# Optimization experiments

Hardware: AMD Instinct MI355X
Metric: run time of the kernel (lower is better)

Reference implementation:

```python
import jax, jax.numpy as jnp
import numpy as np

N_QUBITS = 14
N_LAYERS = 2          # n_ansatz_layers
N_TIMESTEPS = 4
DEGREE = 2
N_ROTS = 4 * N_QUBITS * N_LAYERS  # 448 rotation params per qnode call
DIM = 2 ** N_QUBITS
BSZ = 256
STATE_DIM = 4
OUT_DIM = 2


def apply_ry(state, wire, theta):
    # state: (B, 2^n) complex64; theta: (B,) float. Wire 0 = most significant bit (PennyLane convention).
    L, R = 2 ** wire, 2 ** (N_QUBITS - wire - 1)
    st = state.reshape(-1, L, 2, R)
    c = jnp.cos(theta * 0.5)[:, None, None]
    s = jnp.sin(theta * 0.5)[:, None, None]
    s0, s1 = st[:, :, 0, :], st[:, :, 1, :]
    new = jnp.stack([c * s0 - s * s1, s * s0 + c * s1], axis=2)
    return new.reshape(state.shape)


def apply_crx(state, ctrl, tgt, theta):
    # Controlled-RX: RX(theta) on tgt when ctrl bit is 1.
    a, b = (ctrl, tgt) if ctrl < tgt else (tgt, ctrl)
    La, Lm, Lr = 2 ** a, 2 ** (b - a - 1), 2 ** (N_QUBITS - b - 1)
    st = state.reshape(-1, La, 2, Lm, 2, Lr)
    c = jnp.cos(theta * 0.5)[:, None, None, None]
    s = jnp.sin(theta * 0.5)[:, None, None, None]
    if ctrl < tgt:
        # axis2 = ctrl, axis4 = tgt
        ctl1 = st[:, :, 1]                      # (B, La, Lm, 2, Lr)
        t0, t1 = ctl1[:, :, :, 0, :], ctl1[:, :, :, 1, :]
        n0 = c * t0 - 1j * s * t1
        n1 = -1j * s * t0 + c * t1
        new_ctl1 = jnp.stack([n0, n1], axis=3)
        out = jnp.stack([st[:, :, 0], new_ctl1], axis=2)
    else:
        # axis2 = tgt, axis4 = ctrl
        t0c1, t1c1 = st[:, :, 0, :, 1, :], st[:, :, 1, :, 1, :]
        n0 = c * t0c1 - 1j * s * t1c1
        n1 = -1j * s * t0c1 + c * t1c1
        new_t0 = jnp.stack([st[:, :, 0, :, 0, :], n0], axis=3)
        new_t1 = jnp.stack([st[:, :, 1, :, 0, :], n1], axis=3)
        out = jnp.stack([new_t0, new_t1], axis=2)
    return out.reshape(state.shape)


def sim14(state, params):
    # sim14_circuit: per layer -> RY ring, descending CRX ring [i,(i+1)%n], RY ring, CRX ring [i,(i-1)%n].
    idx = 0
    for _ in range(N_LAYERS):
        for i in range(N_QUBITS):
            state = apply_ry(state, i, params[:, idx]); idx += 1
        for i in range(N_QUBITS - 1, -1, -1):
            state = apply_crx(state, i, (i + 1) % N_QUBITS, params[:, idx]); idx += 1
        for i in range(N_QUBITS):
            state = apply_ry(state, i, params[:, idx]); idx += 1
        for i in [N_QUBITS - 1] + list(range(N_QUBITS - 1)):
            state = apply_crx(state, i, (i - 1) % N_QUBITS, params[:, idx]); idx += 1
    return state


def poly_state(base, tparams, mix_coeffs, poly_coeffs):
    # evaluate_polynomial_state_pl: degree+1 rounds of timestep-mixed circuit outputs.
    result = jnp.zeros_like(base)
    for d in range(DEGREE + 1):
        mixed = jnp.zeros_like(base)
        for t in range(N_TIMESTEPS):
            mixed = mixed + mix_coeffs[:, t:t + 1] * sim14(base, tparams[:, t, :])
        result = result + poly_coeffs[d] * mixed
        if d < DEGREE:
            nrm = jnp.linalg.norm(mixed, axis=1, keepdims=True)
            base = mixed / (nrm + 1e-9)
    return result


def expval_z(state, wire):
    L, R = 2 ** wire, 2 ** (N_QUBITS - wire - 1)
    st = state.reshape(-1, L, 2, R)
    p = jnp.sum(jnp.abs(st) ** 2, axis=(1, 3))  # (B, 2)
    return p[:, 0] - p[:, 1]


def setup_inputs() -> dict:
    key = jax.random.key(0)
    ks = jax.random.split(key, 7)
    return {
        "x": jax.random.normal(ks[0], (BSZ, STATE_DIM), dtype=jnp.float32),
        "W_in": jax.random.normal(ks[1], (STATE_DIM, N_TIMESTEPS * N_ROTS), dtype=jnp.float32) * 0.3,
        "b_in": jax.random.normal(ks[2], (N_TIMESTEPS * N_ROTS,), dtype=jnp.float32) * 0.1,
        "mix_coeffs": jax.random.normal(ks[3], (1, N_TIMESTEPS), dtype=jnp.float32) * 0.5,
        "poly_coeffs": jax.random.normal(ks[4], (DEGREE + 1,), dtype=jnp.float32) * 0.5,
        "W_out": jax.random.normal(ks[5], (N_QUBITS, OUT_DIM), dtype=jnp.float32) * 0.3,
        "b_out": jax.random.normal(ks[6], (OUT_DIM,), dtype=jnp.float32) * 0.1,
    }


def reference(x, W_in, b_in, mix_coeffs, poly_coeffs, W_out, b_out):
    bsz = x.shape[0]
    # v1-style sigmoid [0,1] angle scaling
    angles = jax.nn.sigmoid(x @ W_in + b_in)                # (B, T*n_rots)
    tparams = angles.reshape(bsz, N_TIMESTEPS, N_ROTS)
    base = jnp.zeros((bsz, DIM), dtype=jnp.complex64).at[:, 0].set(1.0)
    final = poly_state(base, tparams, mix_coeffs, poly_coeffs)
    final = final / (jnp.linalg.norm(final, axis=1, keepdims=True) + 1e-9)
    expz = jnp.stack([expval_z(final, w) for w in range(N_QUBITS)], axis=1)  # (B, n_qubits) real
    return expz.astype(jnp.float32) @ W_out + b_out
```

## Files before the change

### kernel.cpp

```cpp
#include <hip/hip_runtime.h>
#include <math.h>

#define DIM 16384
#define NTH 512
#define NBLK 256
#define F4 (DIM / 2)

typedef float v2f __attribute__((ext_vector_type(2)));
typedef float v4f __attribute__((ext_vector_type(4)));

__host__ __device__ constexpr int cswz(int i) {
  return i ^ ((i >> 4) & 15) ^ ((i >> 8) & 15) ^ ((i >> 12) & 3);
}

constexpr int LW[8][5] = {
  {13, 12, 11, 10, 0}, {10, 9, 8, 7, 6}, {6, 5, 4, 3, 2}, {2, 1, 0, 3, 4},
  {12, 13, 0, 1, 2}, {2, 3, 4, 5, 6}, {6, 7, 8, 9, 10}, {10, 11, 12, 13, 9},
};
constexpr int PMAP[8][9] = {
  {4, 5, 6, 7, 8, 9, 10, 11, 12}, {0, 1, 2, 11, 8, 9, 10, 12, 13},
  {0, 1, 2, 3, 4, 5, 6, 12, 13}, {0, 1, 2, 3, 4, 5, 6, 7, 8},
  {2, 3, 4, 5, 6, 7, 8, 9, 10}, {0, 1, 2, 3, 4, 5, 6, 12, 13},
  {0, 1, 2, 11, 8, 9, 10, 12, 13}, {5, 6, 7, 8, 9, 10, 11, 12, 13},
};
constexpr int NG[8] = {9, 8, 8, 3, 9, 8, 8, 3};
constexpr int GATES[8][9][4] = {
  {{0,4,0,0},{0,3,0,10},{0,2,0,11},{0,1,0,12},{0,0,0,13},{1,0,4,14},{1,1,0,15},{1,2,1,16},{1,3,2,17}},
  {{0,4,0,6},{0,3,0,7},{0,2,0,8},{0,1,0,9},{1,1,0,18},{1,2,1,19},{1,3,2,20},{1,4,3,21},{0,0,0,0}},
  {{0,4,0,2},{0,3,0,3},{0,2,0,4},{0,1,0,5},{1,1,0,22},{1,2,1,23},{1,3,2,24},{1,4,3,25},{0,0,0,0}},
  {{0,1,0,1},{1,1,0,26},{1,2,1,27},{0,0,0,0},{0,0,0,0},{0,0,0,0},{0,0,0,0},{0,0,0,0},{0,0,0,0}},
  {{0,2,0,28},{0,3,0,29},{0,4,0,30},{0,0,0,40},{0,1,0,41},{1,1,0,42},{1,2,1,43},{1,3,2,44},{1,4,3,45}},
  {{0,1,0,31},{0,2,0,32},{0,3,0,33},{0,4,0,34},{1,1,0,46},{1,2,1,47},{1,3,2,48},{1,4,3,49},{0,0,0,0}},
  {{0,1,0,35},{0,2,0,36},{0,3,0,37},{0,4,0,38},{1,1,0,50},{1,2,1,51},{1,3,2,52},{1,4,3,53},{0,0,0,0}},
  {{0,1,0,39},{1,1,0,54},{1,2,1,55},{0,0,0,0},{0,0,0,0},{0,0,0,0},{0,0,0,0},{0,0,0,0},{0,0,0,0}},
};
__host__ __device__ constexpr int offcube5(int p, int j) {
  int o = 0;
  for (int b = 0; b < 5; ++b)
    if ((j >> b) & 1) o |= 1 << (13 - LW[p][b]);
  return o;
}

template <int PID, int MODE>
__device__ __forceinline__ void fb_pass(v2f* __restrict__ S, const v2f* __restrict__ CS,
                                        int lb, int tid, v2f* __restrict__ a) {
  int base = 0;
#pragma unroll
  for (int k = 0; k < 9; ++k) base |= ((tid >> k) & 1) << PMAP[PID][k];
  const int sb = cswz(base);
  if (MODE == 1) {
#pragma unroll
    for (int j = 0; j < 32; ++j) a[j] = v2f{0.f, 0.f};
    if (tid == 0) a[0] = v2f{1.f, 0.f};
  } else {
#pragma unroll
    for (int j = 0; j < 32; ++j) a[j] = S[sb ^ cswz(offcube5(PID, j))];
  }
#pragma unroll
  for (int g = 0; g < NG[PID]; ++g) {
    const v2f cs2 = CS[lb + GATES[PID][g][3]];
    const float c = cs2.x, s = cs2.y;
    if (GATES[PID][g][0] == 0) {
      const int tb = GATES[PID][g][1];
#pragma unroll
      for (int j = 0; j < 32; ++j)
        if (!((j >> tb) & 1)) {
          const int j2 = j | (1 << tb);
          const v2f a0 = a[j], a1 = a[j2];
          a[j]  = c * a0 - s * a1;
          a[j2] = s * a0 + c * a1;
        }
    } else {
      const int bc = GATES[PID][g][1], bt = GATES[PID][g][2];
#pragma unroll
      for (int j = 0; j < 32; ++j)
        if (((j >> bc) & 1) && !((j >> bt) & 1)) {
          const int j2 = j | (1 << bt);
          const v2f t0 = a[j], t1 = a[j2];
          a[j]  = c * t0 + s * v2f{t1.y, -t1.x};
          a[j2] = c * t1 + s * v2f{t0.y, -t0.x};
        }
    }
  }
  if (MODE != 2) {
#pragma unroll
    for (int j = 0; j < 32; ++j) S[sb ^ cswz(offcube5(PID, j))] = a[j];
  }
  __syncthreads();
}

__device__ __forceinline__ void sim16(v2f* __restrict__ S, const v2f* __restrict__ CS,
                                      int tid, bool init0) {
  v2f a[32];
  if (init0) fb_pass<0, 1>(S, CS, 0, tid, a);
  else       fb_pass<0, 0>(S, CS, 0, tid, a);
  fb_pass<1, 0>(S, CS, 0, tid, a);
  fb_pass<2, 0>(S, CS, 0, tid, a);
  fb_pass<3, 0>(S, CS, 0, tid, a);
  fb_pass<4, 0>(S, CS, 0, tid, a);
  fb_pass<5, 0>(S, CS, 0, tid, a);
  fb_pass<6, 0>(S, CS, 0, tid, a);
  fb_pass<7, 0>(S, CS, 0, tid, a);
  fb_pass<0, 0>(S, CS, 56, tid, a);
  fb_pass<1, 0>(S, CS, 56, tid, a);
  fb_pass<2, 0>(S, CS, 56, tid, a);
  fb_pass<3, 0>(S, CS, 56, tid, a);
  fb_pass<4, 0>(S, CS, 56, tid, a);
  fb_pass<5, 0>(S, CS, 56, tid, a);
  fb_pass<6, 0>(S, CS, 56, tid, a);
  fb_pass<7, 0>(S, CS, 56, tid, a);
}

__device__ __forceinline__ float block_sum(float v, int tid, float* red) {
#pragma unroll
  for (int off = 32; off; off >>= 1) v += __shfl_xor(v, off);
  if ((tid & 63) == 0) red[tid >> 6] = v;
  __syncthreads();
  float tot = 0.f;
#pragma unroll
  for (int w = 0; w < 8; ++w) tot += red[w];
  __syncthreads();
  return tot;
}

__global__ __launch_bounds__(NTH, 1) void qts_kernel(
    const float* __restrict__ x, const float* __restrict__ Win,
    const float* __restrict__ bin, const float* __restrict__ mix,
    const float* __restrict__ poly, const float* __restrict__ Wout,
    const float* __restrict__ bout, float* __restrict__ out,
    v4f* __restrict__ gAall, v4f* __restrict__ gBall) {
  __shared__ v2f S[DIM + 448 + 128];
  v4f* SF = (v4f*)S;
  v2f* CSall = S + DIM;
  float* red = (float*)(S + DIM + 448);
  const int tid = threadIdx.x;
  const int b = blockIdx.x;
  v4f* gA = gAall + (size_t)b * F4;
  v4f* gB = gBall + (size_t)b * F4;

  if (tid < 448) {
    float z = bin[tid];
    const float x0 = x[b * 4 + 0], x1 = x[b * 4 + 1], x2 = x[b * 4 + 2], x3 = x[b * 4 + 3];
    z += x0 * Win[tid] + x1 * Win[448 + tid] + x2 * Win[896 + tid] + x3 * Win[1344 + tid];
    const float th = 1.f / (1.f + expf(-z));
    float sn, cc;
    sincosf(0.5f * th, &sn, &cc);
    CSall[tid] = v2f{cc, sn};
  }
  __syncthreads();

  const float p0 = poly[0], p1 = poly[1], p2 = poly[2];
  float n1 = 0.f, n2 = 0.f;

  for (int t = 0; t < 4; ++t) {
    sim16(S, CSall + t * 112, tid, true);
    const float mc = mix[t];
    if (t == 0) {
#pragma unroll
      for (int j = 0; j < 16; ++j) { const int f = tid + j * NTH; gA[f] = mc * SF[f]; }
    } else if (t < 3) {
#pragma unroll
      for (int j = 0; j < 16; ++j) { const int f = tid + j * NTH; gA[f] += mc * SF[f]; }
    } else {
      float part = 0.f;
#pragma unroll
      for (int j = 0; j < 16; ++j) {
        const int f = tid + j * NTH;
        const v4f v = gA[f] + mc * SF[f];
        gA[f] = v; SF[f] = v;
        part += v.x * v.x + v.y * v.y + v.z * v.z + v.w * v.w;
      }
      n1 = sqrtf(block_sum(part, tid, red));
    }
    __syncthreads();
  }
  const float n1e = n1 + 1e-9f;
  const float c2 = p1 / n1e;

  for (int t = 0; t < 4; ++t) {
    sim16(S, CSall + t * 112, tid, false);
    const float mc = mix[t];
    if (t == 0) {
#pragma unroll
      for (int j = 0; j < 16; ++j) {
        const int f = tid + j * NTH;
        gB[f] = mc * SF[f]; SF[f] = gA[f];
      }
    } else if (t < 3) {
#pragma unroll
      for (int j = 0; j < 16; ++j) {
        const int f = tid + j * NTH;
        gB[f] += mc * SF[f]; SF[f] = gA[f];
      }
    } else {
      float part = 0.f;
#pragma unroll
      for (int j = 0; j < 16; ++j) {
        const int f = tid + j * NTH;
        const v4f v = gB[f] + mc * SF[f];
        gB[f] = v;
        gA[f] = p0 * gA[f] + c2 * v;
        SF[f] = v;
        part += v.x * v.x + v.y * v.y + v.z * v.z + v.w * v.w;
      }
      n2 = sqrtf(block_sum(part, tid, red));
    }
    __syncthreads();
  }
  const float n2e = n2 + 1e-9f * n1e;
  const float c3 = p2 / n2e;

  float part15[15];
#pragma unroll
  for (int v = 0; v < 15; ++v) part15[v] = 0.f;
  for (int t = 0; t < 4; ++t) {
    sim16(S, CSall + t * 112, tid, false);
    const float mc = c3 * mix[t];
    if (t < 3) {
#pragma unroll
      for (int j = 0; j < 16; ++j) {
        const int f = tid + j * NTH;
        gA[f] += mc * SF[f]; SF[f] = gB[f];
      }
      __syncthreads();
    } else {
#pragma unroll
      for (int j = 0; j < 16; ++j) {
        const int f = tid + j * NTH;
        const v4f r = gA[f] + mc * SF[f];
        const int i0 = cswz(2 * f);
        const int i1 = i0 ^ 1;
        const float pa = r.x * r.x + r.y * r.y;
        const float pb = r.z * r.z + r.w * r.w;
        part15[14] += pa + pb;
#pragma unroll
        for (int w = 0; w < 14; ++w) {
          part15[w] += ((i0 >> (13 - w)) & 1) ? -pa : pa;
          part15[w] += ((i1 >> (13 - w)) & 1) ? -pb : pb;
        }
      }
      __syncthreads();
    }
  }

#pragma unroll
  for (int v = 0; v < 15; ++v) {
    float xv = part15[v];
#pragma unroll
    for (int off = 32; off; off >>= 1) xv += __shfl_xor(xv, off);
    if ((tid & 63) == 0) red[(tid >> 6) * 15 + v] = xv;
  }
  __syncthreads();
  if (tid < 15) {
    float tot = 0.f;
#pragma unroll
    for (int w = 0; w < 8; ++w) tot += red[w * 15 + tid];
    red[128 + tid] = tot;
  }
  __syncthreads();
  if (tid < 2) {
    const float nrm = sqrtf(red[128 + 14]) + 1e-9f;
    const float iv = 1.f / (nrm * nrm);
    float o = bout[tid];
#pragma unroll
    for (int w = 0; w < 14; ++w) o += red[128 + w] * iv * Wout[w * 2 + tid];
    out[b * 2 + tid] = o;
  }
}

__device__ __forceinline__ void fb_sim(v2f* __restrict__ S, const v2f* __restrict__ CS,
                                       int tid, v2f* __restrict__ a,
                                       const v2f* __restrict__ basev, int own_sb,
                                       bool initzero) {
  if (initzero) {
    fb_pass<0, 1>(S, CS, 0, tid, a);
  } else {
#pragma unroll
    for (int j = 0; j < 32; ++j) S[own_sb ^ cswz(offcube5(7, j))] = basev[j];
    __syncthreads();
    fb_pass<0, 0>(S, CS, 0, tid, a);
  }
  fb_pass<1, 0>(S, CS, 0, tid, a);
  fb_pass<2, 0>(S, CS, 0, tid, a);
  fb_pass<3, 0>(S, CS, 0, tid, a);
  fb_pass<4, 0>(S, CS, 0, tid, a);
  fb_pass<5, 0>(S, CS, 0, tid, a);
  fb_pass<6, 0>(S, CS, 0, tid, a);
  fb_pass<7, 0>(S, CS, 0, tid, a);
  fb_pass<0, 0>(S, CS, 56, tid, a);
  fb_pass<1, 0>(S, CS, 56, tid, a);
  fb_pass<2, 0>(S, CS, 56, tid, a);
  fb_pass<3, 0>(S, CS, 56, tid, a);
  fb_pass<4, 0>(S, CS, 56, tid, a);
  fb_pass<5, 0>(S, CS, 56, tid, a);
  fb_pass<6, 0>(S, CS, 56, tid, a);
  fb_pass<7, 2>(S, CS, 56, tid, a);
}
__global__ __launch_bounds__(NTH, 1) void qts_fb(
    const float* __restrict__ x, const float* __restrict__ Win,
    const float* __restrict__ bin, const float* __restrict__ mix,
    const float* __restrict__ poly, const float* __restrict__ Wout,
    const float* __restrict__ bout, float* __restrict__ out) {
  __shared__ v2f S[DIM + 448 + 128];
  v2f* CSall = S + DIM;
  float* red = (float*)(S + DIM + 448);
  const int tid = threadIdx.x;
  const int b = blockIdx.x;
  if (tid < 448) {
    float z = bin[tid];
    const float x0 = x[b * 4 + 0], x1 = x[b * 4 + 1], x2 = x[b * 4 + 2], x3 = x[b * 4 + 3];
    z += x0 * Win[tid] + x1 * Win[448 + tid] + x2 * Win[896 + tid] + x3 * Win[1344 + tid];
    const float th = 1.f / (1.f + expf(-z));
    float sn, cc;
    sincosf(0.5f * th, &sn, &cc);
    CSall[tid] = v2f{cc, sn};
  }
  __syncthreads();
  int ownbase = 0;
#pragma unroll
  for (int k = 0; k < 9; ++k) ownbase |= ((tid >> k) & 1) << PMAP[7][k];
  const int own_sb = cswz(ownbase);
  const float p0 = poly[0], p1 = poly[1], p2 = poly[2];
  v2f a[32], acc[32], basev[32];
  float alpha;
#pragma unroll
  for (int j = 0; j < 32; ++j) acc[j] = v2f{0.f, 0.f};
  for (int t = 0; t < 4; ++t) {
    fb_sim(S, CSall + t * 112, tid, a, basev, own_sb, true);
    const float mc = mix[t];
#pragma unroll
    for (int j = 0; j < 32; ++j) acc[j] += mc * a[j];
  }
  {
    float part = 0.f;
#pragma unroll
    for (int j = 0; j < 32; ++j) part += acc[j].x * acc[j].x + acc[j].y * acc[j].y;
    const float tot = block_sum(part, tid, red);
    const float nu = sqrtf(tot) + 1e-9f;
    const float inv = 1.f / nu;
    alpha = p0 * nu;
#pragma unroll
    for (int j = 0; j < 32; ++j) { basev[j] = inv * acc[j]; acc[j] = v2f{0.f, 0.f}; }
  }
  for (int t = 0; t < 4; ++t) {
    fb_sim(S, CSall + t * 112, tid, a, basev, own_sb, false);
    const float mc = mix[t];
#pragma unroll
    for (int j = 0; j < 32; ++j) acc[j] += mc * a[j];
  }
  {
    float part = 0.f;
#pragma unroll
    for (int j = 0; j < 32; ++j) part += acc[j].x * acc[j].x + acc[j].y * acc[j].y;
    const float tot = block_sum(part, tid, red);
    const float nu = sqrtf(tot) + 1e-9f;
    const float inv = 1.f / nu;
#pragma unroll
    for (int j = 0; j < 32; ++j) {
      const v2f tmp = acc[j];
      acc[j] = alpha * basev[j] + p1 * tmp;
      basev[j] = inv * tmp;
    }
  }
  for (int t = 0; t < 4; ++t) {
    fb_sim(S, CSall + t * 112, tid, a, basev, own_sb, false);
    const float mc = p2 * mix[t];
#pragma unroll
    for (int j = 0; j < 32; ++j) acc[j] += mc * a[j];
  }
  float part[15];
#pragma unroll
  for (int v = 0; v < 15; ++v) part[v] = 0.f;
#pragma unroll
  for (int j = 0; j < 32; ++j) {
    const int idx = ownbase | offcube5(7, j);
    const float p = acc[j].x * acc[j].x + acc[j].y * acc[j].y;
    part[14] += p;
#pragma unroll
    for (int w = 0; w < 14; ++w) part[w] += ((idx >> (13 - w)) & 1) ? -p : p;
  }
  __syncthreads();
#pragma unroll
  for (int v = 0; v < 15; ++v) {
    float xv = part[v];
#pragma unroll
    for (int off = 32; off; off >>= 1) xv += __shfl_xor(xv, off);
    if ((tid & 63) == 0) red[(tid >> 6) * 15 + v] = xv;
  }
  __syncthreads();
  if (tid < 15) {
    float tot = 0.f;
#pragma unroll
    for (int w = 0; w < 8; ++w) tot += red[w * 15 + tid];
    red[128 + tid] = tot;
  }
  __syncthreads();
  if (tid < 2) {
    const float nrm = sqrtf(red[128 + 14]) + 1e-9f;
    const float iv = 1.f / (nrm * nrm);
    float o = bout[tid];
#pragma unroll
    for (int w = 0; w < 14; ++w) o += red[128 + w] * iv * Wout[w * 2 + tid];
    out[b * 2 + tid] = o;
  }
}

extern "C" void kernel_launch(void* const* d_in, const int* in_sizes, int n_in,
                              void* d_out, int out_size, void* d_ws, size_t ws_size,
                              hipStream_t stream) {
  const float* x    = (const float*)d_in[0];
  const float* Win  = (const float*)d_in[1];
  const float* bin  = (const float*)d_in[2];
  const float* mix  = (const float*)d_in[3];
  const float* poly = (const float*)d_in[4];
  const float* Wout = (const float*)d_in[5];
  const float* bout = (const float*)d_in[6];
  float* out = (float*)d_out;

  const size_t need = 2ull * NBLK * F4 * sizeof(v4f);
  if (ws_size >= need) {
    v4f* gA = (v4f*)d_ws;
    v4f* gB = gA + (size_t)NBLK * F4;
    qts_kernel<<<NBLK, NTH, 0, stream>>>(x, Win, bin, mix, poly, Wout, bout, out, gA, gB);
  } else {
    qts_fb<<<NBLK, NTH, 0, stream>>>(x, Win, bin, mix, poly, Wout, bout, out);
  }
}
```

Before: 967.1 us.

## Use 1024 threads per block with 4-qubit register passes in main kernel

The main kernel now runs 1024 threads per block. Each thread holds 16 amplitudes (4 local qubits) instead of 32 (5 local qubits), and the gate schedule is regrouped into 10 passes per layer instead of 8. This raises wave-level parallelism per CU and lowers register pressure, since only one block of 256 fits each CU. The cost is more shared-memory round trips and more __syncthreads barriers per circuit. The fallback kernel keeps the old 512-thread, 5-qubit scheme under renamed tables.

Result: no change. 962.6 us (-0.5%).

```diff
diff --git a/kernel.cpp b/kernel.cpp
--- a/kernel.cpp
+++ b/kernel.cpp
@@ -2,9 +2,10 @@
 #include <math.h>
 
 #define DIM 16384
-#define NTH 512
+#define NTH 1024
 #define NBLK 256
 #define F4 (DIM / 2)
+#define IT4 (F4 / NTH)
 
 typedef float v2f __attribute__((ext_vector_type(2)));
 typedef float v4f __attribute__((ext_vector_type(4)));
@@ -13,57 +14,66 @@
   return i ^ ((i >> 4) & 15) ^ ((i >> 8) & 15) ^ ((i >> 12) & 3);
 }
 
-constexpr int LW[8][5] = {
-  {13, 12, 11, 10, 0}, {10, 9, 8, 7, 6}, {6, 5, 4, 3, 2}, {2, 1, 0, 3, 4},
-  {12, 13, 0, 1, 2}, {2, 3, 4, 5, 6}, {6, 7, 8, 9, 10}, {10, 11, 12, 13, 9},
+constexpr int LWp[10][4] = {
+  {13, 0, 12, 11}, {10, 9, 8, 11}, {7, 6, 5, 8}, {4, 3, 2, 5}, {1, 0, 2, 3},
+  {13, 12, 0, 1}, {2, 1, 3, 4}, {5, 4, 6, 7}, {8, 7, 9, 10}, {11, 10, 12, 9},
 };
-constexpr int PMAP[8][9] = {
-  {4, 5, 6, 7, 8, 9, 10, 11, 12}, {0, 1, 2, 11, 8, 9, 10, 12, 13},
-  {0, 1, 2, 3, 4, 5, 6, 12, 13}, {0, 1, 2, 3, 4, 5, 6, 7, 8},
-  {2, 3, 4, 5, 6, 7, 8, 9, 10}, {0, 1, 2, 3, 4, 5, 6, 12, 13},
-  {0, 1, 2, 11, 8, 9, 10, 12, 13}, {5, 6, 7, 8, 9, 10, 11, 12, 13},
+constexpr int PM[10][10] = {
+  {3, 4, 5, 6, 7, 8, 9, 10, 11, 12},
+  {0, 1, 6, 7, 8, 9, 10, 11, 12, 13},
+  {0, 1, 2, 3, 4, 9, 10, 11, 12, 13},
+  {0, 1, 2, 3, 4, 5, 6, 7, 12, 13},
+  {0, 1, 2, 3, 4, 5, 6, 7, 8, 9},
+  {2, 3, 4, 5, 6, 7, 8, 9, 10, 11},
+  {0, 1, 2, 3, 4, 5, 6, 7, 8, 13},
+  {0, 1, 2, 3, 4, 5, 10, 11, 12, 13},
+  {0, 1, 2, 7, 8, 9, 10, 11, 12, 13},
+  {0, 5, 6, 7, 8, 9, 10, 11, 12, 13},
 };
-constexpr int NG[8] = {9, 8, 8, 3, 9, 8, 8, 3};
-constexpr int GATES[8][9][4] = {
-  {{0,4,0,0},{0,3,0,10},{0,2,0,11},{0,1,0,12},{0,0,0,13},{1,0,4,14},{1,1,0,15},{1,2,1,16},{1,3,2,17}},
-  {{0,4,0,6},{0,3,0,7},{0,2,0,8},{0,1,0,9},{1,1,0,18},{1,2,1,19},{1,3,2,20},{1,4,3,21},{0,0,0,0}},
-  {{0,4,0,2},{0,3,0,3},{0,2,0,4},{0,1,0,5},{1,1,0,22},{1,2,1,23},{1,3,2,24},{1,4,3,25},{0,0,0,0}},
-  {{0,1,0,1},{1,1,0,26},{1,2,1,27},{0,0,0,0},{0,0,0,0},{0,0,0,0},{0,0,0,0},{0,0,0,0},{0,0,0,0}},
-  {{0,2,0,28},{0,3,0,29},{0,4,0,30},{0,0,0,40},{0,1,0,41},{1,1,0,42},{1,2,1,43},{1,3,2,44},{1,4,3,45}},
-  {{0,1,0,31},{0,2,0,32},{0,3,0,33},{0,4,0,34},{1,1,0,46},{1,2,1,47},{1,3,2,48},{1,4,3,49},{0,0,0,0}},
-  {{0,1,0,35},{0,2,0,36},{0,3,0,37},{0,4,0,38},{1,1,0,50},{1,2,1,51},{1,3,2,52},{1,4,3,53},{0,0,0,0}},
-  {{0,1,0,39},{1,1,0,54},{1,2,1,55},{0,0,0,0},{0,0,0,0},{0,0,0,0},{0,0,0,0},{0,0,0,0},{0,0,0,0}},
+constexpr int NGp[10] = {7, 6, 6, 6, 3, 7, 6, 6, 6, 3};
+constexpr int GT[10][7][4] = {
+  {{0,0,0,13},{0,1,0,0},{0,2,0,12},{0,3,0,11},{1,0,1,14},{1,2,0,15},{1,3,2,16}},
+  {{0,0,0,10},{0,1,0,9},{0,2,0,8},{1,0,3,17},{1,1,0,18},{1,2,1,19},{0,0,0,0}},
+  {{0,0,0,7},{0,1,0,6},{0,2,0,5},{1,0,3,20},{1,1,0,21},{1,2,1,22},{0,0,0,0}},
+  {{0,0,0,4},{0,1,0,3},{0,2,0,2},{1,0,3,23},{1,1,0,24},{1,2,1,25},{0,0,0,0}},
+  {{0,0,0,1},{1,0,2,26},{1,1,0,27},{0,0,0,0},{0,0,0,0},{0,0,0,0},{0,0,0,0}},
+  {{0,0,0,41},{0,1,0,40},{0,2,0,28},{0,3,0,29},{1,0,1,42},{1,2,0,43},{1,3,2,44}},
+  {{0,0,0,30},{0,2,0,31},{0,3,0,32},{1,0,1,45},{1,2,0,46},{1,3,2,47},{0,0,0,0}},
+  {{0,0,0,33},{0,2,0,34},{0,3,0,35},{1,0,1,48},{1,2,0,49},{1,3,2,50},{0,0,0,0}},
+  {{0,0,0,36},{0,2,0,37},{0,3,0,38},{1,0,1,51},{1,2,0,52},{1,3,2,53},{0,0,0,0}},
+  {{0,0,0,39},{1,0,1,54},{1,2,0,55},{0,0,0,0},{0,0,0,0},{0,0,0,0},{0,0,0,0}},
 };
-__host__ __device__ constexpr int offcube5(int p, int j) {
+__host__ __device__ constexpr int offcube4(int p, int j) {
   int o = 0;
-  for (int b = 0; b < 5; ++b)
-    if ((j >> b) & 1) o |= 1 << (13 - LW[p][b]);
+  for (int b = 0; b < 4; ++b)
+    if ((j >> b) & 1) o |= 1 << (13 - LWp[p][b]);
   return o;
 }
 
 template <int PID, int MODE>
-__device__ __forceinline__ void fb_pass(v2f* __restrict__ S, const v2f* __restrict__ CS,
-                                        int lb, int tid, v2f* __restrict__ a) {
+__device__ __forceinline__ void pass16(v2f* __restrict__ S, const v2f* __restrict__ CS,
+                                       int tid) {
   int base = 0;
 #pragma unroll
-  for (int k = 0; k < 9; ++k) base |= ((tid >> k) & 1) << PMAP[PID][k];
+  for (int k = 0; k < 10; ++k) base |= ((tid >> k) & 1) << PM[PID][k];
   const int sb = cswz(base);
+  v2f a[16];
   if (MODE == 1) {
 #pragma unroll
-    for (int j = 0; j < 32; ++j) a[j] = v2f{0.f, 0.f};
+    for (int j = 0; j < 16; ++j) a[j] = v2f{0.f, 0.f};
     if (tid == 0) a[0] = v2f{1.f, 0.f};
   } else {
 #pragma unroll
-    for (int j = 0; j < 32; ++j) a[j] = S[sb ^ cswz(offcube5(PID, j))];
-  }
-#pragma unroll
-  for (int g = 0; g < NG[PID]; ++g) {
-    const v2f cs2 = CS[lb + GATES[PID][g][3]];
+    for (int j = 0; j < 16; ++j) a[j] = S[sb ^ cswz(offcube4(PID, j))];
+  }
+#pragma unroll
+  for (int g = 0; g < NGp[PID]; ++g) {
+    const v2f cs2 = CS[GT[PID][g][3]];
     const float c = cs2.x, s = cs2.y;
-    if (GATES[PID][g][0] == 0) {
-      const int tb = GATES[PID][g][1];
-#pragma unroll
-      for (int j = 0; j < 32; ++j)
+    if (GT[PID][g][0] == 0) {
+      const int tb = GT[PID][g][1];
+#pragma unroll
+      for (int j = 0; j < 16; ++j)
         if (!((j >> tb) & 1)) {
           const int j2 = j | (1 << tb);
           const v2f a0 = a[j], a1 = a[j2];
@@ -71,9 +81,9 @@
           a[j2] = s * a0 + c * a1;
         }
     } else {
-      const int bc = GATES[PID][g][1], bt = GATES[PID][g][2];
-#pragma unroll
-      for (int j = 0; j < 32; ++j)
+      const int bc = GT[PID][g][1], bt = GT[PID][g][2];
+#pragma unroll
+      for (int j = 0; j < 16; ++j)
         if (((j >> bc) & 1) && !((j >> bt) & 1)) {
           const int j2 = j | (1 << bt);
           const v2f t0 = a[j], t1 = a[j2];
@@ -82,43 +92,46 @@
         }
     }
   }
-  if (MODE != 2) {
-#pragma unroll
-    for (int j = 0; j < 32; ++j) S[sb ^ cswz(offcube5(PID, j))] = a[j];
-  }
-  __syncthreads();
-}
-
-__device__ __forceinline__ void sim16(v2f* __restrict__ S, const v2f* __restrict__ CS,
-                                      int tid, bool init0) {
-  v2f a[32];
-  if (init0) fb_pass<0, 1>(S, CS, 0, tid, a);
-  else       fb_pass<0, 0>(S, CS, 0, tid, a);
-  fb_pass<1, 0>(S, CS, 0, tid, a);
-  fb_pass<2, 0>(S, CS, 0, tid, a);
-  fb_pass<3, 0>(S, CS, 0, tid, a);
-  fb_pass<4, 0>(S, CS, 0, tid, a);
-  fb_pass<5, 0>(S, CS, 0, tid, a);
-  fb_pass<6, 0>(S, CS, 0, tid, a);
-  fb_pass<7, 0>(S, CS, 0, tid, a);
-  fb_pass<0, 0>(S, CS, 56, tid, a);
-  fb_pass<1, 0>(S, CS, 56, tid, a);
-  fb_pass<2, 0>(S, CS, 56, tid, a);
-  fb_pass<3, 0>(S, CS, 56, tid, a);
-  fb_pass<4, 0>(S, CS, 56, tid, a);
-  fb_pass<5, 0>(S, CS, 56, tid, a);
-  fb_pass<6, 0>(S, CS, 56, tid, a);
-  fb_pass<7, 0>(S, CS, 56, tid, a);
-}
-
-__device__ __forceinline__ float block_sum(float v, int tid, float* red) {
+#pragma unroll
+  for (int j = 0; j < 16; ++j) S[sb ^ cswz(offcube4(PID, j))] = a[j];
+  __syncthreads();
+}
+
+template <bool INIT0>
+__device__ __forceinline__ void run_sim(v2f* __restrict__ S, const v2f* __restrict__ CS,
+                                        int tid) {
+  if (INIT0) pass16<0, 1>(S, CS, tid);
+  else       pass16<0, 0>(S, CS, tid);
+  pass16<1, 0>(S, CS, tid);
+  pass16<2, 0>(S, CS, tid);
+  pass16<3, 0>(S, CS, tid);
+  pass16<4, 0>(S, CS, tid);
+  pass16<5, 0>(S, CS, tid);
+  pass16<6, 0>(S, CS, tid);
+  pass16<7, 0>(S, CS, tid);
+  pass16<8, 0>(S, CS, tid);
+  pass16<9, 0>(S, CS, tid);
+  const v2f* C2 = CS + 56;
+  pass16<0, 0>(S, C2, tid);
+  pass16<1, 0>(S, C2, tid);
+  pass16<2, 0>(S, C2, tid);
+  pass16<3, 0>(S, C2, tid);
+  pass16<4, 0>(S, C2, tid);
+  pass16<5, 0>(S, C2, tid);
+  pass16<6, 0>(S, C2, tid);
+  pass16<7, 0>(S, C2, tid);
+  pass16<8, 0>(S, C2, tid);
+  pass16<9, 0>(S, C2, tid);
+}
+
+__device__ __forceinline__ float block_sum16(float v, int tid, float* red) {
 #pragma unroll
   for (int off = 32; off; off >>= 1) v += __shfl_xor(v, off);
   if ((tid & 63) == 0) red[tid >> 6] = v;
   __syncthreads();
   float tot = 0.f;
 #pragma unroll
-  for (int w = 0; w < 8; ++w) tot += red[w];
+  for (int w = 0; w < 16; ++w) tot += red[w];
   __syncthreads();
   return tot;
 }
@@ -153,24 +166,24 @@
   float n1 = 0.f, n2 = 0.f;
 
   for (int t = 0; t < 4; ++t) {
-    sim16(S, CSall + t * 112, tid, true);
+    run_sim<true>(S, CSall + t * 112, tid);
     const float mc = mix[t];
     if (t == 0) {
 #pragma unroll
-      for (int j = 0; j < 16; ++j) { const int f = tid + j * NTH; gA[f] = mc * SF[f]; }
+      for (int j = 0; j < IT4; ++j) { const int f = tid + j * NTH; gA[f] = mc * SF[f]; }
     } else if (t < 3) {
 #pragma unroll
-      for (int j = 0; j < 16; ++j) { const int f = tid + j * NTH; gA[f] += mc * SF[f]; }
+      for (int j = 0; j < IT4; ++j) { const int f = tid + j * NTH; gA[f] += mc * SF[f]; }
     } else {
       float part = 0.f;
 #pragma unroll
-      for (int j = 0; j < 16; ++j) {
+      for (int j = 0; j < IT4; ++j) {
         const int f = tid + j * NTH;
         const v4f v = gA[f] + mc * SF[f];
         gA[f] = v; SF[f] = v;
         part += v.x * v.x + v.y * v.y + v.z * v.z + v.w * v.w;
       }
-      n1 = sqrtf(block_sum(part, tid, red));
+      n1 = sqrtf(block_sum16(part, tid, red));
     }
     __syncthreads();
   }
@@ -178,24 +191,24 @@
   const float c2 = p1 / n1e;
 
   for (int t = 0; t < 4; ++t) {
-    sim16(S, CSall + t * 112, tid, false);
+    run_sim<false>(S, CSall + t * 112, tid);
     const float mc = mix[t];
     if (t == 0) {
 #pragma unroll
-      for (int j = 0; j < 16; ++j) {
+      for (int j = 0; j < IT4; ++j) {
         const int f = tid + j * NTH;
         gB[f] = mc * SF[f]; SF[f] = gA[f];
       }
     } else if (t < 3) {
 #pragma unroll
-      for (int j = 0; j < 16; ++j) {
+      for (int j = 0; j < IT4; ++j) {
         const int f = tid + j * NTH;
         gB[f] += mc * SF[f]; SF[f] = gA[f];
       }
     } else {
       float part = 0.f;
 #pragma unroll
-      for (int j = 0; j < 16; ++j) {
+      for (int j = 0; j < IT4; ++j) {
         const int f = tid + j * NTH;
         const v4f v = gB[f] + mc * SF[f];
         gB[f] = v;
@@ -203,7 +216,7 @@
         SF[f] = v;
         part += v.x * v.x + v.y * v.y + v.z * v.z + v.w * v.w;
       }
-      n2 = sqrtf(block_sum(part, tid, red));
+      n2 = sqrtf(block_sum16(part, tid, red));
     }
     __syncthreads();
   }
@@ -214,18 +227,18 @@
 #pragma unroll
   for (int v = 0; v < 15; ++v) part15[v] = 0.f;
   for (int t = 0; t < 4; ++t) {
-    sim16(S, CSall + t * 112, tid, false);
+    run_sim<false>(S, CSall + t * 112, tid);
     const float mc = c3 * mix[t];
     if (t < 3) {
 #pragma unroll
-      for (int j = 0; j < 16; ++j) {
+      for (int j = 0; j < IT4; ++j) {
         const int f = tid + j * NTH;
         gA[f] += mc * SF[f]; SF[f] = gB[f];
       }
       __syncthreads();
     } else {
 #pragma unroll
-      for (int j = 0; j < 16; ++j) {
+      for (int j = 0; j < IT4; ++j) {
         const int f = tid + j * NTH;
         const v4f r = gA[f] + mc * SF[f];
         const int i0 = cswz(2 * f);
@@ -254,20 +267,106 @@
   if (tid < 15) {
     float tot = 0.f;
 #pragma unroll
-    for (int w = 0; w < 8; ++w) tot += red[w * 15 + tid];
-    red[128 + tid] = tot;
+    for (int w = 0; w < 16; ++w) tot += red[w * 15 + tid];
+    red[240 + tid] = tot;
   }
   __syncthreads();
   if (tid < 2) {
-    const float nrm = sqrtf(red[128 + 14]) + 1e-9f;
+    const float nrm = sqrtf(red[240 + 14]) + 1e-9f;
     const float iv = 1.f / (nrm * nrm);
     float o = bout[tid];
 #pragma unroll
-    for (int w = 0; w < 14; ++w) o += red[128 + w] * iv * Wout[w * 2 + tid];
+    for (int w = 0; w < 14; ++w) o += red[240 + w] * iv * Wout[w * 2 + tid];
     out[b * 2 + tid] = o;
   }
 }
 
+#define FTH 512
+constexpr int LW5[8][5] = {
+  {13, 12, 11, 10, 0}, {10, 9, 8, 7, 6}, {6, 5, 4, 3, 2}, {2, 1, 0, 3, 4},
+  {12, 13, 0, 1, 2}, {2, 3, 4, 5, 6}, {6, 7, 8, 9, 10}, {10, 11, 12, 13, 9},
+};
+constexpr int PMAP5[8][9] = {
+  {4, 5, 6, 7, 8, 9, 10, 11, 12}, {0, 1, 2, 11, 8, 9, 10, 12, 13},
+  {0, 1, 2, 3, 4, 5, 6, 12, 13}, {0, 1, 2, 3, 4, 5, 6, 7, 8},
+  {2, 3, 4, 5, 6, 7, 8, 9, 10}, {0, 1, 2, 3, 4, 5, 6, 12, 13},
+  {0, 1, 2, 11, 8, 9, 10, 12, 13}, {5, 6, 7, 8, 9, 10, 11, 12, 13},
+};
+constexpr int NG5[8] = {9, 8, 8, 3, 9, 8, 8, 3};
+constexpr int GATES5[8][9][4] = {
+  {{0,4,0,0},{0,3,0,10},{0,2,0,11},{0,1,0,12},{0,0,0,13},{1,0,4,14},{1,1,0,15},{1,2,1,16},{1,3,2,17}},
+  {{0,4,0,6},{0,3,0,7},{0,2,0,8},{0,1,0,9},{1,1,0,18},{1,2,1,19},{1,3,2,20},{1,4,3,21},{0,0,0,0}},
+  {{0,4,0,2},{0,3,0,3},{0,2,0,4},{0,1,0,5},{1,1,0,22},{1,2,1,23},{1,3,2,24},{1,4,3,25},{0,0,0,0}},
+  {{0,1,0,1},{1,1,0,26},{1,2,1,27},{0,0,0,0},{0,0,0,0},{0,0,0,0},{0,0,0,0},{0,0,0,0},{0,0,0,0}},
+  {{0,2,0,28},{0,3,0,29},{0,4,0,30},{0,0,0,40},{0,1,0,41},{1,1,0,42},{1,2,1,43},{1,3,2,44},{1,4,3,45}},
+  {{0,1,0,31},{0,2,0,32},{0,3,0,33},{0,4,0,34},{1,1,0,46},{1,2,1,47},{1,3,2,48},{1,4,3,49},{0,0,0,0}},
+  {{0,1,0,35},{0,2,0,36},{0,3,0,37},{0,4,0,38},{1,1,0,50},{1,2,1,51},{1,3,2,52},{1,4,3,53},{0,0,0,0}},
+  {{0,1,0,39},{1,1,0,54},{1,2,1,55},{0,0,0,0},{0,0,0,0},{0,0,0,0},{0,0,0,0},{0,0,0,0},{0,0,0,0}},
+};
+__host__ __device__ constexpr int offcube5(int p, int j) {
+  int o = 0;
+  for (int b = 0; b < 5; ++b)
+    if ((j >> b) & 1) o |= 1 << (13 - LW5[p][b]);
+  return o;
+}
+template <int PID, int MODE>
+__device__ __forceinline__ void fb_pass(v2f* __restrict__ S, const v2f* __restrict__ CS,
+                                        int lb, int tid, v2f* __restrict__ a) {
+  int base = 0;
+#pragma unroll
+  for (int k = 0; k < 9; ++k) base |= ((tid >> k) & 1) << PMAP5[PID][k];
+  const int sb = cswz(base);
+  if (MODE == 1) {
+#pragma unroll
+    for (int j = 0; j < 32; ++j) a[j] = v2f{0.f, 0.f};
+    if (tid == 0) a[0] = v2f{1.f, 0.f};
+  } else {
+#pragma unroll
+    for (int j = 0; j < 32; ++j) a[j] = S[sb ^ cswz(offcube5(PID, j))];
+  }
+#pragma unroll
+  for (int g = 0; g < NG5[PID]; ++g) {
+    const v2f cs2 = CS[lb + GATES5[PID][g][3]];
+    const float c = cs2.x, s = cs2.y;
+    if (GATES5[PID][g][0] == 0) {
+      const int tb = GATES5[PID][g][1];
+#pragma unroll
+      for (int j = 0; j < 32; ++j)
+        if (!((j >> tb) & 1)) {
+          const int j2 = j | (1 << tb);
+          const v2f a0 = a[j], a1 = a[j2];
+          a[j]  = c * a0 - s * a1;
+          a[j2] = s * a0 + c * a1;
+        }
+    } else {
+      const int bc = GATES5[PID][g][1], bt = GATES5[PID][g][2];
+#pragma unroll
+      for (int j = 0; j < 32; ++j)
+        if (((j >> bc) & 1) && !((j >> bt) & 1)) {
+          const int j2 = j | (1 << bt);
+          const v2f t0 = a[j], t1 = a[j2];
+          a[j]  = c * t0 + s * v2f{t1.y, -t1.x};
+          a[j2] = c * t1 + s * v2f{t0.y, -t0.x};
+        }
+    }
+  }
+  if (MODE != 2) {
+#pragma unroll
+    for (int j = 0; j < 32; ++j) S[sb ^ cswz(offcube5(PID, j))] = a[j];
+  }
+  __syncthreads();
+}
+__device__ __forceinline__ float fb_block_sum(float v, int tid, float* red) {
+#pragma unroll
+  for (int off = 32; off; off >>= 1) v += __shfl_xor(v, off);
+  if ((tid & 63) == 0) red[tid >> 6] = v;
+  __syncthreads();
+  float tot = 0.f;
+#pragma unroll
+  for (int w = 0; w < 8; ++w) tot += red[w];
+  __syncthreads();
+  return tot;
+}
 __device__ __forceinline__ void fb_sim(v2f* __restrict__ S, const v2f* __restrict__ CS,
                                        int tid, v2f* __restrict__ a,
                                        const v2f* __restrict__ basev, int own_sb,
@@ -296,7 +395,7 @@
   fb_pass<6, 0>(S, CS, 56, tid, a);
   fb_pass<7, 2>(S, CS, 56, tid, a);
 }
-__global__ __launch_bounds__(NTH, 1) void qts_fb(
+__global__ __launch_bounds__(FTH, 1) void qts_fb(
     const float* __restrict__ x, const float* __restrict__ Win,
     const float* __restrict__ bin, const float* __restrict__ mix,
     const float* __restrict__ poly, const float* __restrict__ Wout,
@@ -318,7 +417,7 @@
   __syncthreads();
   int ownbase = 0;
 #pragma unroll
-  for (int k = 0; k < 9; ++k) ownbase |= ((tid >> k) & 1) << PMAP[7][k];
+  for (int k = 0; k < 9; ++k) ownbase |= ((tid >> k) & 1) << PMAP5[7][k];
   const int own_sb = cswz(ownbase);
   const float p0 = poly[0], p1 = poly[1], p2 = poly[2];
   v2f a[32], acc[32], basev[32];
@@ -335,7 +434,7 @@
     float part = 0.f;
 #pragma unroll
     for (int j = 0; j < 32; ++j) part += acc[j].x * acc[j].x + acc[j].y * acc[j].y;
-    const float tot = block_sum(part, tid, red);
+    const float tot = fb_block_sum(part, tid, red);
     const float nu = sqrtf(tot) + 1e-9f;
     const float inv = 1.f / nu;
     alpha = p0 * nu;
@@ -352,7 +451,7 @@
     float part = 0.f;
 #pragma unroll
     for (int j = 0; j < 32; ++j) part += acc[j].x * acc[j].x + acc[j].y * acc[j].y;
-    const float tot = block_sum(part, tid, red);
+    const float tot = fb_block_sum(part, tid, red);
     const float nu = sqrtf(tot) + 1e-9f;
     const float inv = 1.f / nu;
 #pragma unroll
@@ -423,6 +522,6 @@
     v4f* gB = gA + (size_t)NBLK * F4;
     qts_kernel<<<NBLK, NTH, 0, stream>>>(x, Win, bin, mix, poly, Wout, bout, out, gA, gB);
   } else {
-    qts_fb<<<NBLK, NTH, 0, stream>>>(x, Win, bin, mix, poly, Wout, bout, out);
-  }
-}
+    qts_fb<<<NBLK, FTH, 0, stream>>>(x, Win, bin, mix, poly, Wout, bout, out);
+  }
+}
```
